# Optimization experiments

Measured on AMD Instinct MI355X. Metric: run time of the kernel, lower is better.

The kernel has to match this reference:

```python
import jax, jax.numpy as jnp
import numpy as np

EPS = 1e-9
LDIM = 4  # dim_g + dim_t + dim_b + dim_w


def _mvn_logpdf(v, F):
    # batched zero-mean multivariate normal log-density, v: (N,O), F: (N,O,O)
    chol = jnp.linalg.cholesky(F)
    z = jax.scipy.linalg.solve_triangular(chol, v[..., None], lower=True)[..., 0]
    quad = jnp.sum(z * z, axis=-1)
    logdet = 2.0 * jnp.sum(jnp.log(jnp.diagonal(chol, axis1=-2, axis2=-1)), axis=-1)
    k = v.shape[-1]
    return -0.5 * (quad + logdet + k * jnp.log(2.0 * jnp.pi))


def _forward(y, B_G, B_T, B_B, B_W, lambda_r1_free, lambda_r2_free,
             q_diag, r_diag, gamma1, gamma2_learnable):
    N, Nt, O = y.shape
    L = LDIM
    # ----- _build_matrices -----
    B11 = jnp.zeros((L, L)).at[0, 0].set(B_G[0, 0]).at[1, 1].set(B_T[0, 0]).at[2, 2].set(B_B[0, 0])
    B22 = jnp.zeros((L, L)).at[3, 3].set(B_W[0, 0])
    B12 = jnp.zeros((L, L)).at[3, :3].set(1.0 / 3.0)  # regime1 factors feed shared factor
    B21 = jnp.zeros((L, L))
    L1 = jnp.zeros((O, L))
    L1 = L1.at[0, 0].set(1.0).at[1, 0].set(lambda_r1_free[0]).at[2, 0].set(lambda_r1_free[1])
    L1 = L1.at[3, 1].set(1.0).at[4, 1].set(lambda_r1_free[2]).at[5, 1].set(lambda_r1_free[3])
    L1 = L1.at[6, 2].set(1.0).at[7, 2].set(lambda_r1_free[4]).at[8, 2].set(lambda_r1_free[5])
    L2 = jnp.zeros((O, L)).at[0, 3].set(1.0).at[1:, 3].set(lambda_r2_free)
    Q = jnp.diag(jnp.abs(q_diag) + 1e-4)
    R = jnp.diag(jnp.abs(r_diag) + 1e-4)
    F_JIT = 1e-5 * jnp.eye(O)
    I_L = jnp.eye(L)
    P22_CONST = 0.9999

    # ----- initial beliefs ('informative') -----
    prob0 = jnp.tile(jnp.array([0.99, 0.01], jnp.float32), (N, 1))
    eta0 = jnp.zeros((N, L), y.dtype)
    P0 = jnp.tile(jnp.diag(jnp.array([1000.0, 1000.0, 1000.0, 1e-9], y.dtype))[None], (N, 1, 1))

    def predict(B, eta, P):
        # eta: (N,L), P: (N,L,L)
        return eta @ B.T, jnp.einsum('ij,njk,lk->nil', B, P, B) + Q

    def innov(Lm, e, Pp, y_t):
        v = y_t - e @ Lm.T
        F = jnp.einsum('oi,nij,pj->nop', Lm, Pp, Lm) + R + F_JIT
        return v, F

    def kupdate(e, Pp, Lm, v, F):
        LP = jnp.einsum('oi,nij->noj', Lm, Pp)          # (N,O,L)
        K = jnp.swapaxes(jnp.linalg.solve(F, LP), -1, -2)  # P Lm^T F^{-1}, (N,L,O)
        e_u = e + jnp.einsum('nlo,no->nl', K, v)
        IKL = I_L - K @ Lm                                # (N,L,L)
        P_u = IKL @ Pp @ jnp.swapaxes(IKL, -1, -2) + jnp.einsum('nlo,op,nmp->nlm', K, R, K)
        return e_u, P_u

    def collapse(w_a, w_b, e_a, e_b, P_a, P_b):
        e = w_a[:, None] * e_a + w_b[:, None] * e_b
        da, db = e_a - e, e_b - e
        P = (w_a[:, None, None] * (P_a + da[:, :, None] * da[:, None, :])
             + w_b[:, None, None] * (P_b + db[:, :, None] * db[:, None, :]))
        return e, P

    def step(carry, y_t):
        prob, eta1, eta2, P1, P2, ll = carry
        # HMM transition: p11 depends on regime-1 state (first L-1 components)
        logit_p11 = gamma1 + eta1[:, :3] @ gamma2_learnable
        p11 = jax.nn.sigmoid(logit_p11)
        # predictions for the 4 regime transitions (origin -> destination)
        e11, Pp11 = predict(B11, eta1, P1)
        e12, Pp12 = predict(B21, eta2, P2)
        e21, Pp21 = predict(B12, eta1, P1)
        e22, Pp22 = predict(B22, eta2, P2)
        v11, F11 = innov(L1, e11, Pp11, y_t)
        v12, F12 = innov(L1, e12, Pp12, y_t)
        v21, F21 = innov(L2, e21, Pp21, y_t)
        v22, F22 = innov(L2, e22, Pp22, y_t)
        ll11 = _mvn_logpdf(v11, F11)
        ll12 = _mvn_logpdf(v12, F12)
        ll21 = _mvn_logpdf(v21, F21)
        ll22 = _mvn_logpdf(v22, F22)
        lp = jnp.log(prob + EPS)
        c11 = lp[:, 0] + jnp.log(p11 + EPS) + ll11
        c12 = lp[:, 1] + np.log(1.0 - P22_CONST + EPS) + ll12
        c21 = lp[:, 0] + jnp.log(1.0 - p11 + EPS) + ll21
        c22 = lp[:, 1] + np.log(P22_CONST + EPS) + ll22
        logp = jnp.stack([c11, c12, c21, c22], axis=1)
        ll_t = jax.scipy.special.logsumexp(logp, axis=1)
        pt = jnp.exp(logp - ll_t[:, None])
        pr1 = pt[:, 0] + pt[:, 1]
        pr2 = pt[:, 2] + pt[:, 3]
        W11 = pt[:, 0] / (pr1 + EPS)
        W12 = pt[:, 1] / (pr1 + EPS)
        W21 = pt[:, 2] / (pr2 + EPS)
        W22 = pt[:, 3] / (pr2 + EPS)
        eu11, Pu11 = kupdate(e11, Pp11, L1, v11, F11)
        eu12, Pu12 = kupdate(e12, Pp12, L1, v12, F12)
        eu21, Pu21 = kupdate(e21, Pp21, L2, v21, F21)
        eu22, Pu22 = kupdate(e22, Pp22, L2, v22, F22)
        eta1n, P1n = collapse(W11, W12, eu11, eu12, Pu11, Pu12)
        eta2n, P2n = collapse(W21, W22, eu21, eu22, Pu21, Pu22)
        probn = jnp.stack([pr1, pr2], axis=1)
        return (probn, eta1n, eta2n, P1n, P2n, ll + ll_t.sum()), None

    carry0 = (prob0, eta0, eta0, P0, P0, jnp.zeros((), y.dtype))
    (_, _, _, _, _, total_ll), _ = jax.lax.scan(step, carry0, jnp.swapaxes(y, 0, 1))
    return total_ll


def setup_inputs() -> dict:
    key = jax.random.key(0)
    ks = jax.random.split(key, 12)
    N, Nt, O = 16384, 64, 9
    f32 = jnp.float32
    return {
        'y': jax.random.normal(ks[0], (N, Nt, O), f32),
        'B_G': jax.random.uniform(ks[1], (1, 1), f32, 0.6, 0.95),  # Beta(5,1.5)-like AR coeffs
        'B_T': jax.random.uniform(ks[2], (1, 1), f32, 0.6, 0.95),
        'B_B': jax.random.uniform(ks[3], (1, 1), f32, 0.6, 0.95),
        'B_W': jax.random.uniform(ks[4], (1, 1), f32, 0.6, 0.95),
        'lambda_r1_free': jax.random.normal(ks[5], (6,), f32),
        'lambda_r2_free': jax.random.normal(ks[6], (O - 1,), f32),
        'q_diag': jax.random.uniform(ks[7], (LDIM,), f32),
        'r_diag': jax.random.uniform(ks[8], (O,), f32),
        'gamma1': jnp.abs(jax.random.normal(ks[9], (), f32)),
        'gamma2_learnable': jax.random.normal(ks[10], (LDIM - 1,), f32),
    }


def reference(y, B_G, B_T, B_B, B_W, lambda_r1_free, lambda_r2_free,
              q_diag, r_diag, gamma1, gamma2_learnable):
    return _forward(y, B_G, B_T, B_B, B_W, lambda_r1_free, lambda_r2_free,
                    q_diag, r_diag, gamma1, gamma2_learnable)
```

## Files before the change

### kernel.cpp

```cpp
#include <hip/hip_runtime.h>


static __device__ __forceinline__ float frcp(float x) { return __builtin_amdgcn_rcpf(x); }

#define NLOG2PI    16.540893597684108f
#define LOG_1M_P22 -9.210330372026184f
#define LOG_P22    -1.00004000233e-4f
#define EPSF       1e-9f
#define LOG_EPS    -20.72326583694641f

__global__ __launch_bounds__(64)
void kf_kernel(const float* __restrict__ y,
               const float* __restrict__ pBG, const float* __restrict__ pBT,
               const float* __restrict__ pBB, const float* __restrict__ pBW,
               const float* __restrict__ lam1, const float* __restrict__ lam2,
               const float* __restrict__ qd,  const float* __restrict__ rd,
               const float* __restrict__ pG1, const float* __restrict__ pG2,
               float* __restrict__ partial, int N, int Nt)
{
    const int lane = threadIdx.x;
    const int n = blockIdx.x * 64 + lane;
    const bool valid = (n < N);
    const int rowlen = Nt * 9;
    const int nchunk = Nt / 4;

    const float bg = pBG[0], bt = pBT[0], bb = pBB[0], bw = pBW[0];
    float a[9], l2v[9], id[9], ad[9], ld[9];
    a[0] = 1.f; a[1] = lam1[0]; a[2] = lam1[1];
    a[3] = 1.f; a[4] = lam1[2]; a[5] = lam1[3];
    a[6] = 1.f; a[7] = lam1[4]; a[8] = lam1[5];
    l2v[0] = 1.f;
    #pragma unroll
    for (int i = 0; i < 8; ++i) l2v[i + 1] = lam2[i];
    float logdetD = 0.f;
    #pragma unroll
    for (int o = 0; o < 9; ++o) {
        float dv = fabsf(rd[o]) + 1.0e-4f + 1.0e-5f;
        id[o] = 1.0f / dv;
        ad[o] = a[o] * id[o];
        ld[o] = l2v[o] * id[o];
        logdetD += __logf(dv);
    }
    const float q0 = fabsf(qd[0]) + 1e-4f, q1 = fabsf(qd[1]) + 1e-4f;
    const float q2 = fabsf(qd[2]) + 1e-4f, q3 = fabsf(qd[3]) + 1e-4f;
    const float g0 = a[0]*ad[0] + a[1]*ad[1] + a[2]*ad[2];
    const float g1 = a[3]*ad[3] + a[4]*ad[4] + a[5]*ad[5];
    const float g2 = a[6]*ad[6] + a[7]*ad[7] + a[8]*ad[8];
    float h = 0.f;
    #pragma unroll
    for (int o = 0; o < 9; ++o) h += l2v[o] * ld[o];
    const float pk0 = q0 / (1.f + q0 * g0);
    const float pk1 = q1 / (1.f + q1 * g1);
    const float pk2 = q2 / (1.f + q2 * g2);
    const float logdet12 = logdetD + __logf((1.f + q0*g0) * (1.f + q1*g1) * (1.f + q2*g2));
    const float gam1 = pG1[0], w0 = pG2[0], w1 = pG2[1], w2 = pG2[2];

    float lp1 = -0.010050326f;
    float lp2 = -4.6051702f;
    float se0 = 0.f, se1 = 0.f, se2 = 0.f;
    float P00 = 1000.f, P01 = 0.f, P02 = 0.f, P11 = 1000.f, P12 = 0.f, P22 = 1000.f;
    float sm2 = 0.f, sp2 = 1e-9f;
    float acc = 0.0f;

    const float* row = y + (size_t)(valid ? n : 0) * rowlen;

    float4 A[9], B[9];
    #pragma unroll
    for (int i = 0; i < 9; ++i) A[i] = *(const float4*)(row + i * 4);

    auto step4 = [&](const float4 (&buf)[9]) {
        #pragma unroll
        for (int s = 0; s < 4; ++s) {
            float yv[9];
            #pragma unroll
            for (int o = 0; o < 9; ++o) {
                const int idx = s * 9 + o, vno = idx >> 2, cm = idx & 3;
                yv[o] = (cm == 0) ? buf[vno].x : (cm == 1) ? buf[vno].y
                      : (cm == 2) ? buf[vno].z : buf[vno].w;
            }

            float logit = gam1 + w0 * se0 + w1 * se1 + w2 * se2;
            float alog = fabsf(logit);
            float lse = __logf(1.0f + __expf(-alog));
            float lp11 = fmaxf(fminf(logit, 0.0f) - lse, LOG_EPS);
            float lm11 = fmaxf(fminf(-logit, 0.0f) - lse, LOG_EPS);

            float ep0 = bg * se0, ep1 = bt * se1, ep2 = bb * se2;
            float S00 = bg*bg*P00 + q0, S01 = bg*bt*P01, S02 = bg*bb*P02;
            float S11 = bt*bt*P11 + q1, S12 = bt*bb*P12, S22 = bb*bb*P22 + q2;
            float v0 = yv[0] - a[0]*ep0, v1 = yv[1] - a[1]*ep0, v2 = yv[2] - a[2]*ep0;
            float v3 = yv[3] - a[3]*ep1, v4 = yv[4] - a[4]*ep1, v5 = yv[5] - a[5]*ep1;
            float v6 = yv[6] - a[6]*ep2, v7 = yv[7] - a[7]*ep2, v8 = yv[8] - a[8]*ep2;
            float u0 = ad[0]*v0 + ad[1]*v1 + ad[2]*v2;
            float u1 = ad[3]*v3 + ad[4]*v4 + ad[5]*v5;
            float u2 = ad[6]*v6 + ad[7]*v7 + ad[8]*v8;
            float vdv = id[0]*v0*v0 + id[1]*v1*v1 + id[2]*v2*v2
                      + id[3]*v3*v3 + id[4]*v4*v4 + id[5]*v5*v5
                      + id[6]*v6*v6 + id[7]*v7*v7 + id[8]*v8*v8;
            float cA = S11*S22 - S12*S12, cB = S02*S12 - S01*S22, cC = S01*S12 - S02*S11;
            float detS = S00*cA + S01*cB + S02*cC;
            float cD = S00*S22 - S02*S02, cE = S01*S02 - S00*S12, cF = S00*S11 - S01*S01;
            float iS = frcp(detS);
            float C00 = cA*iS + g0, C01 = cB*iS, C02 = cC*iS;
            float C11 = cD*iS + g1, C12 = cE*iS, C22 = cF*iS + g2;
            float eA = C11*C22 - C12*C12, eB = C02*C12 - C01*C22, eC = C01*C12 - C02*C11;
            float detC = C00*eA + C01*eB + C02*eC;
            float eD = C00*C22 - C02*C02, eE = C01*C02 - C00*C12, eF = C00*C11 - C01*C01;
            float iC = frcp(detC);
            float Ci00 = eA*iC, Ci01 = eB*iC, Ci02 = eC*iC;
            float Ci11 = eD*iC, Ci12 = eE*iC, Ci22 = eF*iC;
            float t0 = Ci00*u0 + Ci01*u1 + Ci02*u2;
            float t1 = Ci01*u0 + Ci11*u1 + Ci12*u2;
            float t2 = Ci02*u0 + Ci12*u1 + Ci22*u2;
            float quad11 = vdv - (u0*t0 + u1*t1 + u2*t2);
            float ll11 = -0.5f * (quad11 + logdetD + __logf(detS * detC) + NLOG2PI);
            float eu0 = ep0 + t0, eu1 = ep1 + t1, eu2 = ep2 + t2;

            float u120 = u0 + g0*ep0, u121 = u1 + g1*ep1, u122 = u2 + g2*ep2;
            float ydy = vdv + 2.f*(ep0*u0 + ep1*u1 + ep2*u2)
                      + g0*ep0*ep0 + g1*ep1*ep1 + g2*ep2*ep2;
            float quad12 = ydy - (pk0*u120*u120 + pk1*u121*u121 + pk2*u122*u122);
            float ll12 = -0.5f * (quad12 + logdet12 + NLOG2PI);
            float f0 = pk0*u120, f1 = pk1*u121, f2 = pk2*u122;

            float yl = ld[0]*yv[0] + ld[1]*yv[1] + ld[2]*yv[2] + ld[3]*yv[3] + ld[4]*yv[4]
                     + ld[5]*yv[5] + ld[6]*yv[6] + ld[7]*yv[7] + ld[8]*yv[8];
            float m21 = (se0 + se1 + se2) * (1.0f / 3.0f);
            float sP = P00 + P11 + P22 + 2.f*(P01 + P02 + P12);
            float pa = q3 + (1.0f / 9.0f) * sP;
            float m22 = bw * sm2;
            float pb = bw*bw*sp2 + q3;
            float u1a = yl - m21*h;
            float vda = ydy - m21*(2.f*yl - m21*h);
            float dena = 1.f + pa*h;  float idea = frcp(dena);
            float quad21 = vda - pa*u1a*u1a*idea;
            float ll21 = -0.5f * (quad21 + logdetD + __logf(dena) + NLOG2PI);
            float pua = pa*idea;
            float eua = m21 + pua*u1a;
            float u1b = yl - m22*h;
            float vdb = ydy - m22*(2.f*yl - m22*h);
            float denb = 1.f + pb*h;  float ideb = frcp(denb);
            float quad22 = vdb - pb*u1b*u1b*ideb;
            float ll22 = -0.5f * (quad22 + logdetD + __logf(denb) + NLOG2PI);
            float pub = pb*ideb;
            float eub = m22 + pub*u1b;

            float c11 = lp1 + lp11 + ll11;
            float c21 = lp1 + lm11 + ll21;
            float c12 = lp2 + LOG_1M_P22 + ll12;
            float c22 = lp2 + LOG_P22 + ll22;
            float mx = fmaxf(fmaxf(c11, c12), fmaxf(c21, c22));
            float s11 = __expf(c11 - mx), s12 = __expf(c12 - mx);
            float s21 = __expf(c21 - mx), s22 = __expf(c22 - mx);
            float ssum = s11 + s12 + s21 + s22;
            float lss = __logf(ssum);
            acc += mx + lss;
            float pr1n = s11 + s12, pr2n = s21 + s22;
            float den1 = pr1n + EPSF * ssum;
            float den2 = pr2n + EPSF * ssum;
            float inv1 = frcp(den1);
            float inv2 = frcp(den2);
            float W11 = s11 * inv1, W12 = s12 * inv1;
            float W21 = s21 * inv2, W22 = s22 * inv2;
            lp1 = __logf(den1) - lss;
            lp2 = __logf(den2) - lss;

            float ne0 = W11*eu0 + W12*f0;
            float ne1 = W11*eu1 + W12*f1;
            float ne2 = W11*eu2 + W12*f2;
            float da0 = eu0 - ne0, da1 = eu1 - ne1, da2 = eu2 - ne2;
            float db0 = f0 - ne0,  db1 = f1 - ne1,  db2 = f2 - ne2;
            P00 = W11*(Ci00 + da0*da0) + W12*(pk0 + db0*db0);
            P01 = W11*(Ci01 + da0*da1) + W12*(db0*db1);
            P02 = W11*(Ci02 + da0*da2) + W12*(db0*db2);
            P11 = W11*(Ci11 + da1*da1) + W12*(pk1 + db1*db1);
            P12 = W11*(Ci12 + da1*da2) + W12*(db1*db2);
            P22 = W11*(Ci22 + da2*da2) + W12*(pk2 + db2*db2);
            se0 = ne0; se1 = ne1; se2 = ne2;

            float nm2 = W21*eua + W22*eub;
            float dc = eua - nm2, dd = eub - nm2;
            sp2 = W21*(pua + dc*dc) + W22*(pub + dd*dd);
            sm2 = nm2;
        }
    };

    for (int c = 0; c < nchunk; c += 2) {
        {
            const float* p = row + min(c + 1, nchunk - 1) * 36;
            #pragma unroll
            for (int i = 0; i < 9; ++i) B[i] = *(const float4*)(p + i * 4);
        }
        step4(A);
        {
            const float* p = row + min(c + 2, nchunk - 1) * 36;
            #pragma unroll
            for (int i = 0; i < 9; ++i) A[i] = *(const float4*)(p + i * 4);
        }
        step4(B);
    }

    if (!valid) acc = 0.0f;
    #pragma unroll
    for (int off = 32; off; off >>= 1) acc += __shfl_down(acc, off, 64);
    if (lane == 0) partial[blockIdx.x] = acc;
}

__global__ __launch_bounds__(64)
void reduce_k(const float* __restrict__ part, float* __restrict__ out, int nb)
{
    float s = 0.f;
    for (int i = threadIdx.x; i < nb; i += 64) s += part[i];
    #pragma unroll
    for (int off = 32; off; off >>= 1) s += __shfl_down(s, off, 64);
    if (threadIdx.x == 0) out[0] = s;
}

extern "C" void kernel_launch(void* const* d_in, const int* in_sizes, int n_in,
                              void* d_out, int out_size, void* d_ws, size_t ws_size,
                              hipStream_t stream)
{
    const float* y    = (const float*)d_in[0];
    const float* pBG  = (const float*)d_in[1];
    const float* pBT  = (const float*)d_in[2];
    const float* pBB  = (const float*)d_in[3];
    const float* pBW  = (const float*)d_in[4];
    const float* lam1 = (const float*)d_in[5];
    const float* lam2 = (const float*)d_in[6];
    const float* qd   = (const float*)d_in[7];
    const float* rd   = (const float*)d_in[8];
    const float* pG1  = (const float*)d_in[9];
    const float* pG2  = (const float*)d_in[10];

    const int total = in_sizes[0];
    const int Nt = 64, O = 9;
    const int N = total / (Nt * O);
    const int blocks = (N + 63) / 64;

    float* partial = (float*)d_ws;
    kf_kernel<<<blocks, 64, 0, stream>>>(y, pBG, pBT, pBB, pBW, lam1, lam2,
                                         qd, rd, pG1, pG2, partial, N, Nt);
    reduce_k<<<1, 64, 0, stream>>>(partial, (float*)d_out, blocks);
}
```

Before: 144.6 us.

## Restructure IMM step math in log2 domain with a single 3x3 inverse

Replaces the two chained 3x3 inversions with one inversion of (I + S G) via its adjugate, which yields both the updated covariance and the log-determinant. All log/exp work moves to the native base-2 instructions. Regime probabilities are carried in linear form rather than as log-probabilities, which removes several logs per step, and the constant log-det terms are hoisted out of the time loop. The prefetch clamp is replaced with a conditional load. Linear-domain probabilities and the reformulated inverse may change numerical behaviour, for example underflow when a regime probability becomes very small.

After: 138.7 us. -4.1%, faster.

```diff
diff --git a/kernel.cpp b/kernel.cpp
--- a/kernel.cpp
+++ b/kernel.cpp
@@ -1,15 +1,18 @@
 #include <hip/hip_runtime.h>
 
 
-static __device__ __forceinline__ float frcp(float x) { return __builtin_amdgcn_rcpf(x); }
-
-#define NLOG2PI    16.540893597684108f
-#define LOG_1M_P22 -9.210330372026184f
-#define LOG_P22    -1.00004000233e-4f
-#define EPSF       1e-9f
-#define LOG_EPS    -20.72326583694641f
-
-__global__ __launch_bounds__(64)
+static __device__ __forceinline__ float frcp(float x)  { return __builtin_amdgcn_rcpf(x); }
+static __device__ __forceinline__ float fexp2(float x) { return __builtin_amdgcn_exp2f(x); }
+static __device__ __forceinline__ float flog2(float x) { return __builtin_amdgcn_logf(x); }
+
+#define EPSF   1e-9f
+#define L2E    1.4426950408889634f
+#define LN2    0.6931471805599453f
+#define L2_2PI_9 23.86346461225016f
+#define C12F   1.00001e-4f
+#define P22F   0.99990001f
+
+__global__ __launch_bounds__(64, 1)
 void kf_kernel(const float* __restrict__ y,
                const float* __restrict__ pBG, const float* __restrict__ pBT,
                const float* __restrict__ pBB, const float* __restrict__ pBW,
@@ -32,14 +35,14 @@
     l2v[0] = 1.f;
     #pragma unroll
     for (int i = 0; i < 8; ++i) l2v[i + 1] = lam2[i];
-    float logdetD = 0.f;
+    float l2detD = 0.f;
     #pragma unroll
     for (int o = 0; o < 9; ++o) {
         float dv = fabsf(rd[o]) + 1.0e-4f + 1.0e-5f;
         id[o] = 1.0f / dv;
         ad[o] = a[o] * id[o];
         ld[o] = l2v[o] * id[o];
-        logdetD += __logf(dv);
+        l2detD += flog2(dv);
     }
     const float q0 = fabsf(qd[0]) + 1e-4f, q1 = fabsf(qd[1]) + 1e-4f;
     const float q2 = fabsf(qd[2]) + 1e-4f, q3 = fabsf(qd[3]) + 1e-4f;
@@ -52,15 +55,15 @@
     const float pk0 = q0 / (1.f + q0 * g0);
     const float pk1 = q1 / (1.f + q1 * g1);
     const float pk2 = q2 / (1.f + q2 * g2);
-    const float logdet12 = logdetD + __logf((1.f + q0*g0) * (1.f + q1*g1) * (1.f + q2*g2));
+    const float K12 = -0.5f * flog2((1.f + q0*g0) * (1.f + q1*g1) * (1.f + q2*g2));
     const float gam1 = pG1[0], w0 = pG2[0], w1 = pG2[1], w2 = pG2[2];
-
-    float lp1 = -0.010050326f;
-    float lp2 = -4.6051702f;
+    const float CC = -0.5f * (l2detD + L2_2PI_9);
+
+    float pf1 = 0.99f + EPSF, pf2 = 0.01f + EPSF;
     float se0 = 0.f, se1 = 0.f, se2 = 0.f;
     float P00 = 1000.f, P01 = 0.f, P02 = 0.f, P11 = 1000.f, P12 = 0.f, P22 = 1000.f;
     float sm2 = 0.f, sp2 = 1e-9f;
-    float acc = 0.0f;
+    float acc2 = 0.0f;
 
     const float* row = y + (size_t)(valid ? n : 0) * rowlen;
 
@@ -80,10 +83,10 @@
             }
 
             float logit = gam1 + w0 * se0 + w1 * se1 + w2 * se2;
-            float alog = fabsf(logit);
-            float lse = __logf(1.0f + __expf(-alog));
-            float lp11 = fmaxf(fminf(logit, 0.0f) - lse, LOG_EPS);
-            float lm11 = fmaxf(fminf(-logit, 0.0f) - lse, LOG_EPS);
+            float esig = fexp2(-logit * L2E);
+            float p11 = frcp(1.f + esig);
+            float pf11 = p11 + EPSF;
+            float pf21 = 1.f - p11 + EPSF;
 
             float ep0 = bg * se0, ep1 = bt * se1, ep2 = bb * se2;
             float S00 = bg*bg*P00 + q0, S01 = bg*bt*P01, S02 = bg*bb*P02;
@@ -97,30 +100,34 @@
             float vdv = id[0]*v0*v0 + id[1]*v1*v1 + id[2]*v2*v2
                       + id[3]*v3*v3 + id[4]*v4*v4 + id[5]*v5*v5
                       + id[6]*v6*v6 + id[7]*v7*v7 + id[8]*v8*v8;
-            float cA = S11*S22 - S12*S12, cB = S02*S12 - S01*S22, cC = S01*S12 - S02*S11;
-            float detS = S00*cA + S01*cB + S02*cC;
-            float cD = S00*S22 - S02*S02, cE = S01*S02 - S00*S12, cF = S00*S11 - S01*S01;
-            float iS = frcp(detS);
-            float C00 = cA*iS + g0, C01 = cB*iS, C02 = cC*iS;
-            float C11 = cD*iS + g1, C12 = cE*iS, C22 = cF*iS + g2;
-            float eA = C11*C22 - C12*C12, eB = C02*C12 - C01*C22, eC = C01*C12 - C02*C11;
-            float detC = C00*eA + C01*eB + C02*eC;
-            float eD = C00*C22 - C02*C02, eE = C01*C02 - C00*C12, eF = C00*C11 - C01*C01;
-            float iC = frcp(detC);
-            float Ci00 = eA*iC, Ci01 = eB*iC, Ci02 = eC*iC;
-            float Ci11 = eD*iC, Ci12 = eE*iC, Ci22 = eF*iC;
+            float M00 = S00*g0 + 1.f, M01 = S01*g1,       M02 = S02*g2;
+            float M10 = S01*g0,       M11 = S11*g1 + 1.f, M12 = S12*g2;
+            float M20 = S02*g0,       M21 = S12*g1,       M22 = S22*g2 + 1.f;
+            float adj00 = M11*M22 - M12*M21, adj01 = M02*M21 - M01*M22, adj02 = M01*M12 - M02*M11;
+            float adj10 = M12*M20 - M10*M22, adj11 = M00*M22 - M02*M20, adj12 = M02*M10 - M00*M12;
+            float adj20 = M10*M21 - M11*M20, adj21 = M01*M20 - M00*M21, adj22 = M00*M11 - M01*M10;
+            float detM = M00*adj00 + M01*adj10 + M02*adj20;
+            float iM = frcp(detM);
+            float N00 = adj00*S00 + adj01*S01 + adj02*S02;
+            float N01 = adj00*S01 + adj01*S11 + adj02*S12;
+            float N02 = adj00*S02 + adj01*S12 + adj02*S22;
+            float N11 = adj10*S01 + adj11*S11 + adj12*S12;
+            float N12 = adj10*S02 + adj11*S12 + adj12*S22;
+            float N22 = adj20*S02 + adj21*S12 + adj22*S22;
+            float Ci00 = N00*iM, Ci01 = N01*iM, Ci02 = N02*iM;
+            float Ci11 = N11*iM, Ci12 = N12*iM, Ci22 = N22*iM;
             float t0 = Ci00*u0 + Ci01*u1 + Ci02*u2;
             float t1 = Ci01*u0 + Ci11*u1 + Ci12*u2;
             float t2 = Ci02*u0 + Ci12*u1 + Ci22*u2;
             float quad11 = vdv - (u0*t0 + u1*t1 + u2*t2);
-            float ll11 = -0.5f * (quad11 + logdetD + __logf(detS * detC) + NLOG2PI);
+            float n2_11 = -0.5f * fmaf(quad11, L2E, flog2(detM));
             float eu0 = ep0 + t0, eu1 = ep1 + t1, eu2 = ep2 + t2;
 
             float u120 = u0 + g0*ep0, u121 = u1 + g1*ep1, u122 = u2 + g2*ep2;
             float ydy = vdv + 2.f*(ep0*u0 + ep1*u1 + ep2*u2)
                       + g0*ep0*ep0 + g1*ep1*ep1 + g2*ep2*ep2;
             float quad12 = ydy - (pk0*u120*u120 + pk1*u121*u121 + pk2*u122*u122);
-            float ll12 = -0.5f * (quad12 + logdet12 + NLOG2PI);
+            float n2_12 = -0.5f * quad12 * L2E + K12;
             float f0 = pk0*u120, f1 = pk1*u121, f2 = pk2*u122;
 
             float yl = ld[0]*yv[0] + ld[1]*yv[1] + ld[2]*yv[2] + ld[3]*yv[3] + ld[4]*yv[4]
@@ -134,36 +141,34 @@
             float vda = ydy - m21*(2.f*yl - m21*h);
             float dena = 1.f + pa*h;  float idea = frcp(dena);
             float quad21 = vda - pa*u1a*u1a*idea;
-            float ll21 = -0.5f * (quad21 + logdetD + __logf(dena) + NLOG2PI);
+            float n2_21 = -0.5f * fmaf(quad21, L2E, flog2(dena));
             float pua = pa*idea;
             float eua = m21 + pua*u1a;
             float u1b = yl - m22*h;
             float vdb = ydy - m22*(2.f*yl - m22*h);
             float denb = 1.f + pb*h;  float ideb = frcp(denb);
             float quad22 = vdb - pb*u1b*u1b*ideb;
-            float ll22 = -0.5f * (quad22 + logdetD + __logf(denb) + NLOG2PI);
+            float n2_22 = -0.5f * fmaf(quad22, L2E, flog2(denb));
             float pub = pb*ideb;
             float eub = m22 + pub*u1b;
 
-            float c11 = lp1 + lp11 + ll11;
-            float c21 = lp1 + lm11 + ll21;
-            float c12 = lp2 + LOG_1M_P22 + ll12;
-            float c22 = lp2 + LOG_P22 + ll22;
-            float mx = fmaxf(fmaxf(c11, c12), fmaxf(c21, c22));
-            float s11 = __expf(c11 - mx), s12 = __expf(c12 - mx);
-            float s21 = __expf(c21 - mx), s22 = __expf(c22 - mx);
-            float ssum = s11 + s12 + s21 + s22;
-            float lss = __logf(ssum);
-            acc += mx + lss;
-            float pr1n = s11 + s12, pr2n = s21 + s22;
+            float M2 = fmaxf(fmaxf(n2_11, n2_12), fmaxf(n2_21, n2_22));
+            float w11 = pf1 * pf11 * fexp2(n2_11 - M2);
+            float w21 = pf1 * pf21 * fexp2(n2_21 - M2);
+            float w12 = pf2 * C12F * fexp2(n2_12 - M2);
+            float w22 = pf2 * P22F * fexp2(n2_22 - M2);
+            float ssum = w11 + w12 + w21 + w22;
+            acc2 += M2 + flog2(ssum);
+            float pr1n = w11 + w12, pr2n = w21 + w22;
             float den1 = pr1n + EPSF * ssum;
             float den2 = pr2n + EPSF * ssum;
             float inv1 = frcp(den1);
             float inv2 = frcp(den2);
-            float W11 = s11 * inv1, W12 = s12 * inv1;
-            float W21 = s21 * inv2, W22 = s22 * inv2;
-            lp1 = __logf(den1) - lss;
-            lp2 = __logf(den2) - lss;
+            float W11 = w11 * inv1, W12 = w12 * inv1;
+            float W21 = w21 * inv2, W22 = w22 * inv2;
+            float issum = frcp(ssum);
+            pf1 = pr1n * issum + EPSF;
+            pf2 = pr2n * issum + EPSF;
 
             float ne0 = W11*eu0 + W12*f0;
             float ne1 = W11*eu1 + W12*f1;
@@ -186,21 +191,21 @@
     };
 
     for (int c = 0; c < nchunk; c += 2) {
-        {
-            const float* p = row + min(c + 1, nchunk - 1) * 36;
+        if (c + 1 < nchunk) {
+            const float* p = row + (c + 1) * 36;
             #pragma unroll
             for (int i = 0; i < 9; ++i) B[i] = *(const float4*)(p + i * 4);
         }
         step4(A);
-        {
-            const float* p = row + min(c + 2, nchunk - 1) * 36;
+        if (c + 2 < nchunk) {
+            const float* p = row + (c + 2) * 36;
             #pragma unroll
             for (int i = 0; i < 9; ++i) A[i] = *(const float4*)(p + i * 4);
         }
         step4(B);
     }
 
-    if (!valid) acc = 0.0f;
+    float acc = valid ? (acc2 + (float)Nt * CC) * LN2 : 0.0f;
     #pragma unroll
     for (int off = 32; off; off >>= 1) acc += __shfl_down(acc, off, 64);
     if (lane == 0) partial[blockIdx.x] = acc;
```
